# Kernel optimization log

Measured on AMD Instinct MI355X. Metric: run time of the kernel, lower is better.

The kernel has to match this reference:

```python
import jax, jax.numpy as jnp
import numpy as np

NG, K, LEN_KEEP = 128, 32, 32  # n_groups, group_size, int(128*(1-0.75))
ENC_HEADS, DEC_HEADS = 12, 16


def _fps(xyz, init, npoint):
    # iterative farthest point sampling; xyz (B,N,3), init (B,) start indices
    B, N, _ = xyz.shape
    def step(carry, _):
        dmin, far = carry
        c = jnp.take_along_axis(xyz, far[:, None, None], axis=1)  # (B,1,3)
        dmin = jnp.minimum(dmin, jnp.sum((xyz - c) ** 2, -1))
        return (dmin, jnp.argmax(dmin, -1)), far
    _, cents = jax.lax.scan(step, (jnp.full((B, N), 1e10, xyz.dtype), init), None, length=npoint)
    return cents.T  # (B, npoint)


def _knn(xyz, cents, k):
    # squared-distance knn (same ordering as euclidean cdist + topk smallest)
    x2 = jnp.sum(xyz * xyz, -1)          # (B,N)
    c2 = jnp.sum(cents * cents, -1)      # (B,M)
    d = c2[:, :, None] + x2[:, None, :] - 2.0 * jnp.einsum('bmc,bnc->bmn', cents, xyz)
    idx = jax.lax.top_k(-d, k)[1]        # (B,M,k)
    return jax.vmap(lambda p, i: p[i])(xyz, idx)  # (B,M,k,3)


def _bn(x, g, b):
    # train-mode BatchNorm1d over (batch, spatial), channel-last x (BM,k,C)
    m = x.mean((0, 1))
    v = x.var((0, 1))
    return (x - m) * jax.lax.rsqrt(v + 1e-5) * g + b


def _ln(x, g, b):
    m = x.mean(-1, keepdims=True)
    v = ((x - m) ** 2).mean(-1, keepdims=True)
    return (x - m) * jax.lax.rsqrt(v + 1e-5) * g + b


def _layer(x, qw, qb, ow, ob, l1g, l1b, f1w, f1b, f2w, f2b, l2g, l2b, nh):
    # post-norm TransformerEncoderLayer (relu FFN, no dropout = eval mode)
    B, S, D = x.shape
    dh = D // nh
    q, k, v = jnp.split(x @ qw.T + qb, 3, axis=-1)
    q = q.reshape(B, S, nh, dh); k = k.reshape(B, S, nh, dh); v = v.reshape(B, S, nh, dh)
    att = jax.nn.softmax(jnp.einsum('bqhd,bkhd->bhqk', q, k) * (1.0 / float(np.sqrt(dh))), axis=-1)
    o = jnp.einsum('bhqk,bkhd->bqhd', att, v).reshape(B, S, D) @ ow.T + ob
    x = _ln(x + o, l1g, l1b)
    f = jax.nn.relu(x @ f1w.T + f1b) @ f2w.T + f2b
    return _ln(x + f, l2g, l2b)


def _stack(x, qw, qb, ow, ob, l1g, l1b, f1w, f1b, f2w, f2b, l2g, l2b, nh):
    for i in range(qw.shape[0]):
        x = _layer(x, qw[i], qb[i], ow[i], ob[i], l1g[i], l1b[i], f1w[i], f1b[i], f2w[i], f2b[i], l2g[i], l2b[i], nh)
    return x


def _forward(xyz, fps_init, ids_shuffle, cw1, cb1, g1, be1, cw2, cb2, g2, be2, cw3, cb3, g3, be3, pos_w, pos_b, eqw, eqb, eow, eob, el1g, el1b, ef1w, ef1b, ef2w, ef2b, el2g, el2b, dew, deb, mtok, dpw, dpb, dqw, dqb, dow, dob, dl1g, dl1b, df1w, df1b, df2w, df2b, dl2g, dl2b, prw, prb):
    B = xyz.shape[0]
    cent_idx = _fps(xyz, fps_init, NG)
    cxyz = jax.vmap(lambda p, i: p[i])(xyz, cent_idx)      # (B,NG,3)
    gn = _knn(xyz, cxyz, K) - cxyz[:, :, None, :]          # (B,NG,K,3) centered groups
    h = gn.reshape(-1, K, 3)
    h = jax.nn.relu(_bn(h @ cw1.T + cb1, g1, be1))
    h = jax.nn.relu(_bn(h @ cw2.T + cb2, g2, be2))
    h = _bn(h @ cw3.T + cb3, g3, be3)
    tokens = h.max(axis=1).reshape(B, NG, -1)              # (B,NG,768)
    x = tokens + cxyz @ pos_w.T + pos_b
    ids_restore = jnp.argsort(ids_shuffle, axis=1)
    xk = jnp.take_along_axis(x, ids_shuffle[:, :LEN_KEEP, None], axis=1)
    mask = jnp.ones((B, NG), xyz.dtype).at[:, :LEN_KEEP].set(0.0)
    mask = jnp.take_along_axis(mask, ids_restore, axis=1)
    lat = _stack(xk, eqw, eqb, eow, eob, el1g, el1b, ef1w, ef1b, ef2w, ef2b, el2g, el2b, ENC_HEADS)
    y = lat @ dew.T + deb
    mt = jnp.broadcast_to(mtok, (B, NG - LEN_KEEP, mtok.shape[0]))
    y_ = jnp.take_along_axis(jnp.concatenate([y, mt], axis=1), ids_restore[:, :, None], axis=1)
    yd = y_ + cxyz @ dpw.T + dpb
    dec = _stack(yd, dqw, dqb, dow, dob, dl1g, dl1b, df1w, df1b, df2w, df2b, dl2g, dl2b, DEC_HEADS)
    pred = dec @ prw.T + prb                               # (B,NG,K*3)
    target = gn.reshape(B, NG, -1)                         # same FPS seed -> same centroids in loss branch
    l = ((pred - target) ** 2).mean(-1)
    loss = (l * mask).sum() / mask.sum()
    return loss, pred, mask


def setup_inputs():
    ks = iter(jax.random.split(jax.random.key(0), 64))
    def W(*shape):
        return jax.random.normal(next(ks), shape, jnp.float32) * 0.02
    B, N, D, DD, Le, Ld = 32, 8192, 768, 512, 12, 8
    d = {}
    d['xyz'] = jax.random.normal(next(ks), (B, N, 3), jnp.float32)
    d['fps_init'] = jax.random.randint(next(ks), (B,), 0, N)
    d['ids_shuffle'] = jnp.argsort(jax.random.uniform(next(ks), (B, NG)), axis=1)
    d['cw1'], d['cb1'], d['g1'], d['be1'] = W(64, 3), jnp.zeros(64), jnp.ones(64), jnp.zeros(64)
    d['cw2'], d['cb2'], d['g2'], d['be2'] = W(128, 64), jnp.zeros(128), jnp.ones(128), jnp.zeros(128)
    d['cw3'], d['cb3'], d['g3'], d['be3'] = W(D, 128), jnp.zeros(D), jnp.ones(D), jnp.zeros(D)
    d['pos_w'], d['pos_b'] = W(D, 3), jnp.zeros(D)
    d['eqw'], d['eqb'] = W(Le, 3 * D, D), jnp.zeros((Le, 3 * D))
    d['eow'], d['eob'] = W(Le, D, D), jnp.zeros((Le, D))
    d['el1g'], d['el1b'] = jnp.ones((Le, D)), jnp.zeros((Le, D))
    d['ef1w'], d['ef1b'] = W(Le, 4 * D, D), jnp.zeros((Le, 4 * D))
    d['ef2w'], d['ef2b'] = W(Le, D, 4 * D), jnp.zeros((Le, D))
    d['el2g'], d['el2b'] = jnp.ones((Le, D)), jnp.zeros((Le, D))
    d['dew'], d['deb'] = W(DD, D), jnp.zeros(DD)
    d['mtok'] = jnp.zeros(DD)
    d['dpw'], d['dpb'] = W(DD, 3), jnp.zeros(DD)
    d['dqw'], d['dqb'] = W(Ld, 3 * DD, DD), jnp.zeros((Ld, 3 * DD))
    d['dow'], d['dob'] = W(Ld, DD, DD), jnp.zeros((Ld, DD))
    d['dl1g'], d['dl1b'] = jnp.ones((Ld, DD)), jnp.zeros((Ld, DD))
    d['df1w'], d['df1b'] = W(Ld, 4 * DD, DD), jnp.zeros((Ld, 4 * DD))
    d['df2w'], d['df2b'] = W(Ld, DD, 4 * DD), jnp.zeros((Ld, DD))
    d['dl2g'], d['dl2b'] = jnp.ones((Ld, DD)), jnp.zeros((Ld, DD))
    d['prw'], d['prb'] = W(K * 3, DD), jnp.zeros(K * 3)
    return d


def reference(xyz, fps_init, ids_shuffle, cw1, cb1, g1, be1, cw2, cb2, g2, be2, cw3, cb3, g3, be3, pos_w, pos_b, eqw, eqb, eow, eob, el1g, el1b, ef1w, ef1b, ef2w, ef2b, el2g, el2b, dew, deb, mtok, dpw, dpb, dqw, dqb, dow, dob, dl1g, dl1b, df1w, df1b, df2w, df2b, dl2g, dl2b, prw, prb):
    return _forward(xyz, fps_init, ids_shuffle, cw1, cb1, g1, be1, cw2, cb2, g2, be2, cw3, cb3, g3, be3, pos_w, pos_b, eqw, eqb, eow, eob, el1g, el1b, ef1w, ef1b, ef2w, ef2b, el2g, el2b, dew, deb, mtok, dpw, dpb, dqw, dqb, dow, dob, dl1g, dl1b, df1w, df1b, df2w, df2b, dl2g, dl2b, prw, prb)
```

## Files before the change

### kernel.cpp

```cpp
#include <hip/hip_runtime.h>
#include <cmath>

#define BB 32
#define NPTS 8192
#define NG 128
#define KNB 32
#define LK 32
#define DE 768
#define DD 512
#define NLE 12
#define NLD 8

typedef __bf16 bf16x8 __attribute__((ext_vector_type(8)));
typedef float  f32x4  __attribute__((ext_vector_type(4)));
typedef unsigned long long u64;

#define WAITV(N) asm volatile("s_waitcnt vmcnt(" #N ")" ::: "memory")

static __device__ __forceinline__ bf16x8 pack8(float4 a, float4 b) {
    bf16x8 h;
    h[0] = (__bf16)a.x; h[1] = (__bf16)a.y; h[2] = (__bf16)a.z; h[3] = (__bf16)a.w;
    h[4] = (__bf16)b.x; h[5] = (__bf16)b.y; h[6] = (__bf16)b.z; h[7] = (__bf16)b.w;
    return h;
}

static __device__ __forceinline__ void gload16(const __bf16* g, __bf16* l) {
    __builtin_amdgcn_global_load_lds(
        (const __attribute__((address_space(1))) void*)g,
        (__attribute__((address_space(3))) void*)l,
        16, 0, 0);
}

static __device__ __forceinline__ unsigned fkey(float f) {
    unsigned u = __float_as_uint(f);
    return ((int)u < 0) ? ~u : (u | 0x80000000u);
}

__global__ __launch_bounds__(512, 1) void fps_kernel(
    const float* __restrict__ xyz, const int* __restrict__ init,
    float* __restrict__ cxyz)
{
#pragma clang fp contract(off)
    const int b = blockIdx.x;
    const float* P = xyz + (size_t)b * NPTS * 3;
    __shared__ float pxs[NPTS], pys[NPTS], pzs[NPTS];
    __shared__ u64 red[2][8];
    const int tid = threadIdx.x;
    float x[16], y[16], z[16], dmin[16];
    #pragma unroll
    for (int k = 0; k < 16; ++k) {
        int n = tid + (k << 9);
        float xx = P[n * 3 + 0], yy = P[n * 3 + 1], zz = P[n * 3 + 2];
        x[k] = xx; y[k] = yy; z[k] = zz;
        pxs[n] = xx; pys[n] = yy; pzs[n] = zz;
        dmin[k] = 1e10f;
    }
    int far = init[b];
    __syncthreads();
    for (int t = 0; t < NG; ++t) {
        float cx = pxs[far], cy = pys[far], cz = pzs[far];
        if (tid == 0) {
            cxyz[(b * NG + t) * 3 + 0] = cx;
            cxyz[(b * NG + t) * 3 + 1] = cy;
            cxyz[(b * NG + t) * 3 + 2] = cz;
        }
        float best = -1.0f; int bi = 0;
        #pragma unroll
        for (int k = 0; k < 16; ++k) {
            int n = tid + (k << 9);
            float dx = x[k] - cx, dy = y[k] - cy, dz = z[k] - cz;
            float d = dx * dx + dy * dy + dz * dz;
            float dm = dmin[k];
            if (d < dm) dm = d;
            dmin[k] = dm;
            if (dm > best) { best = dm; bi = n; }
        }
        u64 key = ((u64)__float_as_uint(best) << 32) | (unsigned)(8191 - bi);
        #pragma unroll
        for (int d = 32; d >= 1; d >>= 1) {
            u64 k2 = __shfl_down(key, d);
            if (k2 > key) key = k2;
        }
        if ((tid & 63) == 0) red[t & 1][tid >> 6] = key;
        __syncthreads();
        u64 kb = red[t & 1][0];
        #pragma unroll
        for (int w = 1; w < 8; ++w) {
            u64 k2 = red[t & 1][w];
            if (k2 > kb) kb = k2;
        }
        far = 8191 - (int)(kb & 0xFFFFFFFFu);
    }
}

__global__ __launch_bounds__(256) void knn_kernel(
    const float* __restrict__ xyz, const float* __restrict__ cxyz,
    float* __restrict__ gn)
{
#pragma clang fp contract(off)
    const int bm = blockIdx.x;
    const int b = bm / NG;
    const float* P = xyz + (size_t)b * NPTS * 3;
    __shared__ u64 cand[512];
    __shared__ u64 tmins[4];
    __shared__ int wcnt[4];
    __shared__ int order[KNB];
    const int tid = threadIdx.x;
    const int wv = tid >> 6, lane = tid & 63;
    const float cx = cxyz[bm * 3 + 0], cy = cxyz[bm * 3 + 1], cz = cxyz[bm * 3 + 2];
    const float c2 = cx * cx + cy * cy + cz * cz;
    unsigned fk[32];
    float bestf = 1e31f; int bi = 1 << 30;
    #pragma unroll
    for (int j = 0; j < 32; ++j) {
        int n = tid + (j << 8);
        float x = P[n * 3 + 0], y = P[n * 3 + 1], z = P[n * 3 + 2];
        float x2 = x * x + y * y + z * z;
        float dt = cx * x + cy * y + cz * z;
        float v = (c2 + x2) - 2.0f * dt;
        fk[j] = fkey(v);
        if (v < bestf) { bestf = v; bi = n; }
    }
    u64 mk = ((u64)fkey(bestf) << 32) | (unsigned)bi;
    {
        u64 v = mk;
        #pragma unroll
        for (int k = 2; k <= 64; k <<= 1) {
            #pragma unroll
            for (int j = k >> 1; j > 0; j >>= 1) {
                u64 o = __shfl_xor(v, j);
                bool up = ((lane & k) == 0);
                bool lower = ((lane & j) == 0);
                u64 mn = (v < o) ? v : o;
                u64 mx = (v < o) ? o : v;
                v = (up == lower) ? mn : mx;
            }
        }
        u64 Tw = __shfl(v, 31);
        if (lane == 0) tmins[wv] = Tw;
    }
    __syncthreads();
    u64 T = tmins[0];
    #pragma unroll
    for (int w = 1; w < 4; ++w) { u64 k2 = tmins[w]; if (k2 < T) T = k2; }
    int c = 0;
    #pragma unroll
    for (int j = 0; j < 32; ++j) {
        u64 key = ((u64)fk[j] << 32) | (unsigned)(tid + (j << 8));
        c += (key <= T) ? 1 : 0;
    }
    int s = c;
    #pragma unroll
    for (int d = 1; d < 64; d <<= 1) {
        int t2 = __shfl_up(s, d);
        if (lane >= d) s += t2;
    }
    int excl = s - c;
    if (lane == 63) wcnt[wv] = s;
    __syncthreads();
    int base = 0;
    for (int w = 0; w < wv; ++w) base += wcnt[w];
    int etot = wcnt[0] + wcnt[1] + wcnt[2] + wcnt[3];

    if (etot <= 512) {
        int pos = base + excl;
        #pragma unroll
        for (int j = 0; j < 32; ++j) {
            u64 key = ((u64)fk[j] << 32) | (unsigned)(tid + (j << 8));
            if (key <= T) cand[pos++] = key;
        }
        __syncthreads();
        for (int si = tid; si < etot; si += 256) {
            u64 my = cand[si];
            int r = 0;
            for (int j2 = 0; j2 < etot; ++j2) r += (cand[j2] < my) ? 1 : 0;
            if (r < KNB) order[r] = (int)(my & 0xFFFFFFFFu);
        }
        __syncthreads();
    } else {
        u64 bk = ~0ull;
        #pragma unroll
        for (int j = 0; j < 32; ++j) {
            u64 key = ((u64)fk[j] << 32) | (unsigned)(tid + (j << 8));
            if (key < bk) bk = key;
        }
        for (int r = 0; r < KNB; ++r) {
            u64 kk = bk;
            #pragma unroll
            for (int dd = 32; dd >= 1; dd >>= 1) {
                u64 k2 = __shfl_down(kk, dd);
                if (k2 < kk) kk = k2;
            }
            if (lane == 0) cand[(r & 1) * 4 + wv] = kk;
            __syncthreads();
            u64 kb = cand[(r & 1) * 4 + 0];
            #pragma unroll
            for (int w = 1; w < 4; ++w) { u64 k2 = cand[(r & 1) * 4 + w]; if (k2 < kb) kb = k2; }
            if (tid == 0) order[r] = (int)(kb & 0xFFFFFFFFu);
            if ((int)(kb & 255u) == tid) {
                int sj = (int)((kb & 0xFFFFFFFFu) >> 8);
                #pragma unroll
                for (int j = 0; j < 32; ++j) if (j == sj) fk[j] = 0xFFFFFFFFu;
                bk = ~0ull;
                #pragma unroll
                for (int j = 0; j < 32; ++j) {
                    u64 key = ((u64)fk[j] << 32) | (unsigned)(tid + (j << 8));
                    if (key < bk) bk = key;
                }
            }
            __syncthreads();
        }
    }
    if (tid < KNB) {
        int n = order[tid];
        gn[((size_t)bm * KNB + tid) * 3 + 0] = P[n * 3 + 0] - cx;
        gn[((size_t)bm * KNB + tid) * 3 + 1] = P[n * 3 + 1] - cy;
        gn[((size_t)bm * KNB + tid) * 3 + 2] = P[n * 3 + 2] - cz;
    }
}

__global__ void cvt_bf16_kernel(const float* __restrict__ src, __bf16* __restrict__ dst, int n8)
{
    int i = blockIdx.x * 256 + threadIdx.x;
    if (i >= n8) return;
    const float4* p = (const float4*)(src + (size_t)i * 8);
    *(bf16x8*)(dst + (size_t)i * 8) = pack8(p[0], p[1]);
}

struct CvtTab {
    const float* src[10];
    __bf16* dst[10];
    int cum[11];
};
__global__ void cvt_multi_kernel(CvtTab t)
{
    int i = blockIdx.x * 256 + threadIdx.x;
    if (i >= t.cum[10]) return;
    int seg = 0;
    #pragma unroll
    for (int k = 1; k < 10; ++k) seg += (i >= t.cum[k]) ? 1 : 0;
    int local = i - t.cum[seg];
    const float4* p = (const float4*)(t.src[seg] + (size_t)local * 8);
    *(bf16x8*)(t.dst[seg] + (size_t)local * 8) = pack8(p[0], p[1]);
}

__global__ void embed1_kernel(const float* __restrict__ gn, const float* __restrict__ w,
                              const float* __restrict__ bias, float* __restrict__ h1)
{
    int i = blockIdx.x * 256 + threadIdx.x;
    if (i >= 131072 * 64) return;
    int r = i >> 6, c = i & 63;
    const float* p = gn + (size_t)r * 3;
    h1[i] = p[0] * w[c * 3 + 0] + p[1] * w[c * 3 + 1] + p[2] * w[c * 3 + 2] + bias[c];
}

template <int C>
__global__ __launch_bounds__(256) void colstats_kernel(const float* __restrict__ X,
                                                       double* __restrict__ st, int Mrows)
{
    constexpr int RL = 256 / C;
    const int c = threadIdx.x % C;
    const int rl = threadIdx.x / C;
    double s = 0.0, s2 = 0.0;
    int rows_per_block = (Mrows + gridDim.x - 1) / gridDim.x;
    int r0 = blockIdx.x * rows_per_block;
    int r1 = min(r0 + rows_per_block, Mrows);
    for (int r = r0 + rl; r < r1; r += RL) {
        float v = X[(size_t)r * C + c];
        s += v; s2 += (double)v * v;
    }
    __shared__ double sh[2][256];
    sh[0][threadIdx.x] = s; sh[1][threadIdx.x] = s2;
    __syncthreads();
    if (rl == 0) {
        for (int j = 1; j < RL; ++j) { s += sh[0][j * C + c]; s2 += sh[1][j * C + c]; }
        atomicAdd(&st[c], s);
        atomicAdd(&st[C + c], s2);
    }
}

__global__ void bn_finalize(const double* __restrict__ st, const float* __restrict__ g,
                            const float* __restrict__ be, float* __restrict__ sc,
                            float* __restrict__ shb, int C)
{
    int c = blockIdx.x * 64 + threadIdx.x;
    if (c >= C) return;
    double m = st[c] / 131072.0;
    double var = st[C + c] / 131072.0 - m * m;
    if (var < 0.0) var = 0.0;
    float rs = rsqrtf((float)var + 1e-5f);
    sc[c] = rs * g[c];
    shb[c] = be[c] - (float)m * rs * g[c];
}

__global__ void bn_apply_bf16(const float* __restrict__ x, const float* __restrict__ sc,
                              const float* __restrict__ shb, __bf16* __restrict__ y,
                              int total, int C)
{
    int i = blockIdx.x * 256 + threadIdx.x;
    if (i >= total) return;
    int c = i % C;
    float v = x[i] * sc[c] + shb[c];
    v = fmaxf(v, 0.0f);
    y[i] = (__bf16)v;
}

template <int BM, int WM, int WN, int DEPTH>
__global__ __launch_bounds__(256) void gemm_bf16(
    const __bf16* __restrict__ A, const __bf16* __restrict__ W,
    const float* __restrict__ bias, float* __restrict__ Cf, __bf16* __restrict__ Cb,
    int M, int N, int K, int Kc, int relu)
{
    constexpr int MR = BM / WM / 16;
    constexpr int NR = 128 / WN / 16;
    constexpr int CA = BM * 8 / 256;
    __shared__ __bf16 As[DEPTH][BM * 64];
    __shared__ __bf16 Ws[DEPTH][128 * 64];
    const int tid = threadIdx.x;
    const int lane = tid & 63;
    const int wave = tid >> 6;
    const int wm = wave / WN, wn = wave % WN;
    const int m0 = blockIdx.y * BM, n0 = blockIdx.x * 128;
    const int kb = blockIdx.z * Kc;

    f32x4 acc[MR][NR] = {};

    auto stage = [&](int buf, int kt) {
        #pragma unroll
        for (int j = 0; j < CA; ++j) {
            int cb = j * 256 + (wave << 6);
            int c  = cb + lane;
            int row = c >> 3;
            int kcs = (c & 7) ^ (row & 7);
            gload16(A + (size_t)(m0 + row) * K + kb + kt + kcs * 8, &As[buf][cb * 8]);
        }
        #pragma unroll
        for (int j = 0; j < 4; ++j) {
            int cb = j * 256 + (wave << 6);
            int c  = cb + lane;
            int row = c >> 3;
            int kcs = (c & 7) ^ (row & 7);
            gload16(W + (size_t)(n0 + row) * K + kb + kt + kcs * 8, &Ws[buf][cb * 8]);
        }
    };
    auto compute = [&](int buf) {
        #pragma unroll
        for (int ks = 0; ks < 2; ++ks) {
            bf16x8 af[MR], bfr[NR];
            int kc = ks * 4 + (lane >> 4);
            #pragma unroll
            for (int i = 0; i < MR; ++i) {
                int rowA = wm * (BM / WM) + i * 16 + (lane & 15);
                af[i] = *(bf16x8*)&As[buf][rowA * 64 + ((kc ^ (rowA & 7)) * 8)];
            }
            #pragma unroll
            for (int j = 0; j < NR; ++j) {
                int rowB = wn * (128 / WN) + j * 16 + (lane & 15);
                bfr[j] = *(bf16x8*)&Ws[buf][rowB * 64 + ((kc ^ (rowB & 7)) * 8)];
            }
            #pragma unroll
            for (int i = 0; i < MR; ++i)
                #pragma unroll
                for (int j = 0; j < NR; ++j)
                    acc[i][j] = __builtin_amdgcn_mfma_f32_16x16x32_bf16(af[i], bfr[j], acc[i][j], 0, 0, 0);
        }
    };

    const int nt = Kc >> 6;
    stage(0, 0);
    if (DEPTH > 2 && nt > 1) stage(1, 64);
    for (int t = 0; t < nt; ++t) {
        int ahead = min(nt - 1, t + DEPTH - 2) - t;
        if (ahead >= 1) { if constexpr (BM == 64) WAITV(6); else WAITV(8); }
        else            WAITV(0);
        __syncthreads();
        if (t + DEPTH - 1 < nt) stage((t + DEPTH - 1) % DEPTH, (t + DEPTH - 1) << 6);
        compute(t % DEPTH);
    }

    float* Co = Cf ? Cf + (size_t)blockIdx.z * M * N : nullptr;
    #pragma unroll
    for (int j = 0; j < NR; ++j) {
        int col = n0 + wn * (128 / WN) + j * 16 + (lane & 15);
        if (col >= N) continue;
        float bv = (blockIdx.z == 0) ? bias[col] : 0.0f;
        #pragma unroll
        for (int i = 0; i < MR; ++i) {
            #pragma unroll
            for (int r = 0; r < 4; ++r) {
                int rowm = m0 + wm * (BM / WM) + i * 16 + (lane >> 4) * 4 + r;
                float v = acc[i][j][r] + bv;
                if (relu) v = fmaxf(v, 0.0f);
                if (Co) Co[(size_t)rowm * N + col] = v;
                if (Cb) Cb[(size_t)rowm * N + col] = (__bf16)v;
            }
        }
    }
}

__global__ __launch_bounds__(256) void embed3_mfma(
    const __bf16* __restrict__ A, const __bf16* __restrict__ W,
    const float* __restrict__ cb3,
    float* __restrict__ gmax, float* __restrict__ gmin, double* __restrict__ st3)
{
    __shared__ __bf16 As[2][128 * 64];
    __shared__ __bf16 Ws[2][128 * 64];
    const int tid = threadIdx.x;
    const int lane = tid & 63;
    const int wave = tid >> 6;
    const int wm = wave >> 1, wn = wave & 1;
    const int m0 = blockIdx.y * 128, n0 = blockIdx.x * 128;
    const int K = 128;

    f32x4 acc[4][4] = {};

    auto stage = [&](int buf, int kt) {
        #pragma unroll
        for (int j = 0; j < 4; ++j) {
            int cb = j * 256 + (wave << 6);
            int c  = cb + lane;
            int row = c >> 3;
            int kcs = (c & 7) ^ (row & 7);
            gload16(A + (size_t)(m0 + row) * K + kt + kcs * 8, &As[buf][cb * 8]);
            gload16(W + (size_t)(n0 + row) * K + kt + kcs * 8, &Ws[buf][cb * 8]);
        }
    };
    auto compute = [&](int buf) {
        #pragma unroll
        for (int ks = 0; ks < 2; ++ks) {
            bf16x8 af[4], bfr[4];
            int kc = ks * 4 + (lane >> 4);
            #pragma unroll
            for (int i = 0; i < 4; ++i) {
                int rowA = wm * 64 + i * 16 + (lane & 15);
                af[i] = *(bf16x8*)&As[buf][rowA * 64 + ((kc ^ (rowA & 7)) * 8)];
                int rowB = wn * 64 + i * 16 + (lane & 15);
                bfr[i] = *(bf16x8*)&Ws[buf][rowB * 64 + ((kc ^ (rowB & 7)) * 8)];
            }
            #pragma unroll
            for (int i = 0; i < 4; ++i)
                #pragma unroll
                for (int j = 0; j < 4; ++j)
                    acc[i][j] = __builtin_amdgcn_mfma_f32_16x16x32_bf16(af[i], bfr[j], acc[i][j], 0, 0, 0);
        }
    };

    stage(0, 0);
    stage(1, 64);
    WAITV(8);
    __syncthreads();
    compute(0);
    WAITV(0);
    __syncthreads();
    compute(1);

    #pragma unroll
    for (int j = 0; j < 4; ++j) {
        int col = n0 + wn * 64 + j * 16 + (lane & 15);
        float bv = cb3[col];
        float stot = 0.0f, s2tot = 0.0f;
        #pragma unroll
        for (int gi = 0; gi < 2; ++gi) {
            float mx = -1e30f, mn = 1e30f, s = 0.0f, s2 = 0.0f;
            #pragma unroll
            for (int ii = 0; ii < 2; ++ii) {
                f32x4 a = acc[gi * 2 + ii][j];
                #pragma unroll
                for (int r = 0; r < 4; ++r) {
                    float v = a[r] + bv;
                    mx = fmaxf(mx, v); mn = fminf(mn, v);
                    s += v; s2 += v * v;
                }
            }
            #pragma unroll
            for (int d = 16; d < 64; d <<= 1) {
                mx = fmaxf(mx, __shfl_xor(mx, d));
                mn = fminf(mn, __shfl_xor(mn, d));
                s  += __shfl_xor(s, d);
                s2 += __shfl_xor(s2, d);
            }
            stot += s; s2tot += s2;
            if (lane < 16) {
                int g = (m0 >> 5) + wm * 2 + gi;
                gmax[(size_t)g * 768 + col] = mx;
                gmin[(size_t)g * 768 + col] = mn;
            }
        }
        if (lane < 16) {
            double* stp = st3 + (size_t)(blockIdx.y & 31) * 1536;
            atomicAdd(&stp[col], (double)stot);
            atomicAdd(&stp[768 + col], (double)s2tot);
        }
    }
}

__global__ void bn3_finalize(const double* __restrict__ st3, const float* __restrict__ g,
                             const float* __restrict__ be, float* __restrict__ a3,
                             float* __restrict__ c3)
{
    int c = blockIdx.x * 256 + threadIdx.x;
    if (c >= 768) return;
    double s = 0.0, s2 = 0.0;
    for (int p = 0; p < 32; ++p) { s += st3[(size_t)p * 1536 + c]; s2 += st3[(size_t)p * 1536 + 768 + c]; }
    double m = s / 131072.0;
    double var = s2 / 131072.0 - m * m;
    if (var < 0.0) var = 0.0;
    float rs = rsqrtf((float)var + 1e-5f);
    a3[c] = rs * g[c];
    c3[c] = be[c] - (float)m * rs * g[c];
}

__global__ void tokens_pos(const float* __restrict__ gmax, const float* __restrict__ gmin,
                           const float* __restrict__ a3, const float* __restrict__ c3,
                           const float* __restrict__ cxyz, const float* __restrict__ posw,
                           const float* __restrict__ posb, const int* __restrict__ restore,
                           float* __restrict__ xe, __bf16* __restrict__ xeb)
{
    int i = blockIdx.x * 256 + threadIdx.x;
    if (i >= 4096 * 768) return;
    int c = i % 768, g = i / 768;
    int r = restore[g];
    if (r >= LK) return;
    float a = a3[c];
    float tok = (a >= 0.0f ? a * gmax[i] : a * gmin[i]) + c3[c];
    float px = cxyz[g * 3 + 0], py = cxyz[g * 3 + 1], pz = cxyz[g * 3 + 2];
    float v = tok + px * posw[c * 3 + 0] + py * posw[c * 3 + 1] + pz * posw[c * 3 + 2] + posb[c];
    int b = g >> 7;
    size_t idx = ((size_t)(b * LK + r)) * DE + c;
    xe[idx] = v;
    xeb[idx] = (__bf16)v;
}

__global__ void restore_kernel(const int* __restrict__ shuffle, int* __restrict__ restore,
                               float* __restrict__ maskv)
{
    int j = blockIdx.x * 256 + threadIdx.x;
    if (j >= BB * NG) return;
    int b = j / NG, p = j % NG;
    int dst = b * NG + shuffle[j];
    restore[dst] = p;
    maskv[dst] = (p < LK) ? 0.0f : 1.0f;
}

__global__ void yd_build(const float* __restrict__ ykp, const int* __restrict__ restore,
                         const float* __restrict__ mtok, const float* __restrict__ cxyz,
                         const float* __restrict__ dpw, const float* __restrict__ dpb,
                         float* __restrict__ xd, __bf16* __restrict__ xdb)
{
    const size_t PS = (size_t)1024 * DD;
    int i = blockIdx.x * 256 + threadIdx.x;
    if (i >= BB * NG * DD) return;
    int c = i % DD;
    int g = i / DD;
    int b = g / NG;
    int r = restore[g];
    float base;
    if (r < LK) {
        size_t o = (size_t)(b * LK + r) * DD + c;
        base = ykp[o] + ykp[PS + o] + ykp[2 * PS + o] + ykp[3 * PS + o];
    } else {
        base = mtok[c];
    }
    float px = cxyz[g * 3 + 0], py = cxyz[g * 3 + 1], pz = cxyz[g * 3 + 2];
    float v = base + px * dpw[c * 3 + 0] + py * dpw[c * 3 + 1] + pz * dpw[c * 3 + 2] + dpb[c];
    xd[i] = v;
    xdb[i] = (__bf16)v;
}

template <int S, int DH, int NH>
__global__ __launch_bounds__(256) void dattn_kernel(const __bf16* __restrict__ qkv,
                                                    __bf16* __restrict__ o, float scale)
{
    constexpr int D = NH * DH;
    constexpr int SQ = DH + 8;
    constexpr int SV = S + 8;
    __shared__ __bf16 Qb[S * SQ];
    __shared__ __bf16 Kb[S * SQ];
    __shared__ __bf16 Vt[DH * SV];
    __shared__ __bf16 Pb[S * SV];
    const int h = blockIdx.x % NH;
    const int b = blockIdx.x / NH;
    const int tid = threadIdx.x;
    const int lane = tid & 63, wv = tid >> 6;
    const __bf16* base = qkv + (size_t)b * S * 3 * D + h * DH;
    for (int i = tid; i < S * (DH / 8); i += 256) {
        int s = i / (DH / 8), c8 = (i % (DH / 8)) * 8;
        const __bf16* rp = base + (size_t)s * 3 * D;
        bf16x8 q = *(const bf16x8*)(rp + c8);
        bf16x8 k = *(const bf16x8*)(rp + D + c8);
        bf16x8 v = *(const bf16x8*)(rp + 2 * D + c8);
        *(bf16x8*)&Qb[s * SQ + c8] = q;
        *(bf16x8*)&Kb[s * SQ + c8] = k;
        #pragma unroll
        for (int j = 0; j < 8; ++j) Vt[(c8 + j) * SV + s] = v[j];
    }
    __syncthreads();
    const int q0 = wv * 32;
    const int arow = lane & 15;
    const int kch = (lane >> 4) * 8;
    const int rrow = (lane >> 4) * 4;
    f32x4 sc[2][8];
    {
        bf16x8 af0 = *(bf16x8*)&Qb[(q0 + arow) * SQ + kch];
        bf16x8 af1 = *(bf16x8*)&Qb[(q0 + 16 + arow) * SQ + kch];
        f32x4 z = {0.0f, 0.0f, 0.0f, 0.0f};
        #pragma unroll
        for (int j = 0; j < 8; ++j) {
            bf16x8 bf_ = *(bf16x8*)&Kb[(j * 16 + arow) * SQ + kch];
            sc[0][j] = __builtin_amdgcn_mfma_f32_16x16x32_bf16(af0, bf_, z, 0, 0, 0);
            sc[1][j] = __builtin_amdgcn_mfma_f32_16x16x32_bf16(af1, bf_, z, 0, 0, 0);
        }
    }
    #pragma unroll
    for (int i = 0; i < 2; ++i) {
        #pragma unroll
        for (int r = 0; r < 4; ++r) {
            float m = -1e30f;
            #pragma unroll
            for (int j = 0; j < 8; ++j) m = fmaxf(m, sc[i][j][r]);
            #pragma unroll
            for (int d = 8; d >= 1; d >>= 1) m = fmaxf(m, __shfl_xor(m, d));
            float sum = 0.0f;
            #pragma unroll
            for (int j = 0; j < 8; ++j) {
                float e = expf((sc[i][j][r] - m) * scale);
                sc[i][j][r] = e;
                sum += e;
            }
            #pragma unroll
            for (int d = 8; d >= 1; d >>= 1) sum += __shfl_xor(sum, d);
            float inv = 1.0f / sum;
            int row = q0 + i * 16 + rrow + r;
            #pragma unroll
            for (int j = 0; j < 8; ++j)
                Pb[row * SV + j * 16 + (lane & 15)] = (__bf16)(sc[i][j][r] * inv);
        }
    }
    #pragma unroll
    for (int i = 0; i < 2; ++i) {
        #pragma unroll
        for (int j2 = 0; j2 < 2; ++j2) {
            f32x4 a2 = {0.0f, 0.0f, 0.0f, 0.0f};
            #pragma unroll
            for (int ks = 0; ks < 4; ++ks) {
                bf16x8 pa = *(bf16x8*)&Pb[(q0 + i * 16 + arow) * SV + ks * 32 + kch];
                bf16x8 vb = *(bf16x8*)&Vt[(j2 * 16 + arow) * SV + ks * 32 + kch];
                a2 = __builtin_amdgcn_mfma_f32_16x16x32_bf16(pa, vb, a2, 0, 0, 0);
            }
            #pragma unroll
            for (int r = 0; r < 4; ++r) {
                int q = q0 + i * 16 + rrow + r;
                o[((size_t)(b * S + q)) * D + h * DH + j2 * 16 + (lane & 15)] = (__bf16)a2[r];
            }
        }
    }
}

template <int S, int DH, int NH>
__global__ __launch_bounds__(64) void eattn_kernel(const __bf16* __restrict__ qkv,
                                                   __bf16* __restrict__ o, float scale)
{
    constexpr int D = NH * DH;
    constexpr int SQ = DH + 8;
    constexpr int SV = S + 8;
    __shared__ __bf16 Qb[S * SQ];
    __shared__ __bf16 Kb[S * SQ];
    __shared__ __bf16 Vt[DH * SV];
    __shared__ __bf16 Pb[S * SV];
    const int h = blockIdx.x % NH;
    const int b = blockIdx.x / NH;
    const int lane = threadIdx.x;
    const __bf16* base = qkv + (size_t)b * S * 3 * D + h * DH;
    for (int i = lane; i < S * (DH / 8); i += 64) {
        int s = i / (DH / 8), c8 = (i % (DH / 8)) * 8;
        const __bf16* rp = base + (size_t)s * 3 * D;
        bf16x8 q = *(const bf16x8*)(rp + c8);
        bf16x8 k = *(const bf16x8*)(rp + D + c8);
        bf16x8 v = *(const bf16x8*)(rp + 2 * D + c8);
        *(bf16x8*)&Qb[s * SQ + c8] = q;
        *(bf16x8*)&Kb[s * SQ + c8] = k;
        #pragma unroll
        for (int j = 0; j < 8; ++j) Vt[(c8 + j) * SV + s] = v[j];
    }
    __syncthreads();
    const int arow = lane & 15;
    const int kch = (lane >> 4) * 8;
    const int rrow = (lane >> 4) * 4;
    f32x4 sc[2][2] = {};
    #pragma unroll
    for (int ks = 0; ks < 2; ++ks) {
        bf16x8 af0 = *(bf16x8*)&Qb[(arow) * SQ + ks * 32 + kch];
        bf16x8 af1 = *(bf16x8*)&Qb[(16 + arow) * SQ + ks * 32 + kch];
        #pragma unroll
        for (int j = 0; j < 2; ++j) {
            bf16x8 bf_ = *(bf16x8*)&Kb[(j * 16 + arow) * SQ + ks * 32 + kch];
            sc[0][j] = __builtin_amdgcn_mfma_f32_16x16x32_bf16(af0, bf_, sc[0][j], 0, 0, 0);
            sc[1][j] = __builtin_amdgcn_mfma_f32_16x16x32_bf16(af1, bf_, sc[1][j], 0, 0, 0);
        }
    }
    #pragma unroll
    for (int i = 0; i < 2; ++i) {
        #pragma unroll
        for (int r = 0; r < 4; ++r) {
            float m = fmaxf(sc[i][0][r], sc[i][1][r]);
            #pragma unroll
            for (int d = 8; d >= 1; d >>= 1) m = fmaxf(m, __shfl_xor(m, d));
            float sum = 0.0f;
            #pragma unroll
            for (int j = 0; j < 2; ++j) {
                float e = expf((sc[i][j][r] - m) * scale);
                sc[i][j][r] = e;
                sum += e;
            }
            #pragma unroll
            for (int d = 8; d >= 1; d >>= 1) sum += __shfl_xor(sum, d);
            float inv = 1.0f / sum;
            int row = i * 16 + rrow + r;
            #pragma unroll
            for (int j = 0; j < 2; ++j)
                Pb[row * SV + j * 16 + (lane & 15)] = (__bf16)(sc[i][j][r] * inv);
        }
    }
    __syncthreads();
    #pragma unroll
    for (int i = 0; i < 2; ++i) {
        bf16x8 pa = *(bf16x8*)&Pb[(i * 16 + arow) * SV + kch];
        #pragma unroll
        for (int j2 = 0; j2 < 4; ++j2) {
            bf16x8 vb = *(bf16x8*)&Vt[(j2 * 16 + arow) * SV + kch];
            f32x4 z = {0.0f, 0.0f, 0.0f, 0.0f};
            f32x4 a2 = __builtin_amdgcn_mfma_f32_16x16x32_bf16(pa, vb, z, 0, 0, 0);
            #pragma unroll
            for (int r = 0; r < 4; ++r) {
                int q = i * 16 + rrow + r;
                o[((size_t)(b * S + q)) * D + h * DH + j2 * 16 + (lane & 15)] = (__bf16)a2[r];
            }
        }
    }
}

template <int D, int SK>
__global__ __launch_bounds__(256) void ln_res(float* __restrict__ x, const float* __restrict__ part,
                                              size_t pstride,
                                              const float* __restrict__ g, const float* __restrict__ b,
                                              __bf16* __restrict__ xb)
{
    constexpr int J = D / 256;
    __shared__ float pr[2][4];
    const size_t off = (size_t)blockIdx.x * D;
    const int tid = threadIdx.x;
    float vals[J];
    float s = 0.0f, s2 = 0.0f;
    #pragma unroll
    for (int j = 0; j < J; ++j) {
        int i = tid + j * 256;
        float v = x[off + i];
        #pragma unroll
        for (int sk = 0; sk < SK; ++sk) v += part[(size_t)sk * pstride + off + i];
        vals[j] = v; s += v; s2 += v * v;
    }
    #pragma unroll
    for (int d = 32; d >= 1; d >>= 1) { s += __shfl_down(s, d); s2 += __shfl_down(s2, d); }
    if ((tid & 63) == 0) { pr[0][tid >> 6] = s; pr[1][tid >> 6] = s2; }
    __syncthreads();
    float st = pr[0][0] + pr[0][1] + pr[0][2] + pr[0][3];
    float s2t = pr[1][0] + pr[1][1] + pr[1][2] + pr[1][3];
    float m = st / D;
    float var = s2t / D - m * m;
    if (var < 0.0f) var = 0.0f;
    float rs = rsqrtf(var + 1e-5f);
    #pragma unroll
    for (int j = 0; j < J; ++j) {
        int i = tid + j * 256;
        float v = (vals[j] - m) * rs * g[i] + b[i];
        x[off + i] = v;
        xb[off + i] = (__bf16)v;
    }
}

__global__ __launch_bounds__(128) void loss_l(const float* __restrict__ predp,
                                              const float* __restrict__ target,
                                              const float* __restrict__ maskv,
                                              float* __restrict__ pred_out,
                                              float* __restrict__ lm)
{
    const size_t PS = (size_t)4096 * 96;
    const int g = blockIdx.x;
    __shared__ float red[128];
    int t = threadIdx.x;
    float s = 0.0f;
    if (t < 96) {
        size_t o = (size_t)g * 96 + t;
        float v = predp[o] + predp[PS + o] + predp[2 * PS + o] + predp[3 * PS + o];
        pred_out[o] = v;
        float d = v - target[o];
        s = d * d;
    }
    red[t] = s; __syncthreads();
    for (int st = 64; st > 0; st >>= 1) { if (t < st) red[t] += red[t + st]; __syncthreads(); }
    if (t == 0) lm[g] = (red[0] / 96.0f) * maskv[g];
}

__global__ __launch_bounds__(1024) void loss_final(const float* __restrict__ lm,
                                                   const float* __restrict__ maskv,
                                                   float* __restrict__ out)
{
    __shared__ float r1[1024], r2[1024];
    int t = threadIdx.x;
    float a = 0.0f, b = 0.0f;
    for (int i = t; i < BB * NG; i += 1024) { a += lm[i]; b += maskv[i]; }
    r1[t] = a; r2[t] = b; __syncthreads();
    for (int st = 512; st > 0; st >>= 1) { if (t < st) { r1[t] += r1[t + st]; r2[t] += r2[t + st]; } __syncthreads(); }
    if (t == 0) out[0] = r1[0] / r2[0];
}

extern "C" void kernel_launch(void* const* d_in, const int* in_sizes, int n_in,
                              void* d_out, int out_size, void* d_ws, size_t ws_size,
                              hipStream_t stream)
{
    (void)in_sizes; (void)n_in; (void)out_size; (void)ws_size;
    const float* xyz        = (const float*)d_in[0];
    const int*   fps_init   = (const int*)d_in[1];
    const int*   ids_shuf   = (const int*)d_in[2];
    const float* cw1 = (const float*)d_in[3];  const float* cb1 = (const float*)d_in[4];
    const float* g1  = (const float*)d_in[5];  const float* be1 = (const float*)d_in[6];
    const float* cw2 = (const float*)d_in[7];  const float* cb2 = (const float*)d_in[8];
    const float* g2  = (const float*)d_in[9];  const float* be2 = (const float*)d_in[10];
    const float* cw3 = (const float*)d_in[11]; const float* cb3 = (const float*)d_in[12];
    const float* g3  = (const float*)d_in[13]; const float* be3 = (const float*)d_in[14];
    const float* posw = (const float*)d_in[15]; const float* posb = (const float*)d_in[16];
    const float* eqw = (const float*)d_in[17]; const float* eqb = (const float*)d_in[18];
    const float* eow = (const float*)d_in[19]; const float* eob = (const float*)d_in[20];
    const float* el1g = (const float*)d_in[21]; const float* el1b = (const float*)d_in[22];
    const float* ef1w = (const float*)d_in[23]; const float* ef1b = (const float*)d_in[24];
    const float* ef2w = (const float*)d_in[25]; const float* ef2b = (const float*)d_in[26];
    const float* el2g = (const float*)d_in[27]; const float* el2b = (const float*)d_in[28];
    const float* dew = (const float*)d_in[29]; const float* deb = (const float*)d_in[30];
    const float* mtok = (const float*)d_in[31];
    const float* dpw = (const float*)d_in[32]; const float* dpb = (const float*)d_in[33];
    const float* dqw = (const float*)d_in[34]; const float* dqb = (const float*)d_in[35];
    const float* dow = (const float*)d_in[36]; const float* dob = (const float*)d_in[37];
    const float* dl1g = (const float*)d_in[38]; const float* dl1b = (const float*)d_in[39];
    const float* df1w = (const float*)d_in[40]; const float* df1b = (const float*)d_in[41];
    const float* df2w = (const float*)d_in[42]; const float* df2b = (const float*)d_in[43];
    const float* dl2g = (const float*)d_in[44]; const float* dl2b = (const float*)d_in[45];
    const float* prw = (const float*)d_in[46]; const float* prb = (const float*)d_in[47];
    float* out = (float*)d_out;
    float* pred = out + 1;
    float* maskv = out + 1 + (size_t)BB * NG * KNB * 3;

    char* ws = (char*)d_ws;
    size_t off = 0;
    auto alloc = [&](size_t bytes) -> void* {
        void* p = ws + off;
        off = (off + bytes + 255) & ~(size_t)255;
        return p;
    };
    double* st1 = (double*)alloc(128 * 8);
    double* st2 = (double*)alloc(256 * 8);
    double* st3 = (double*)alloc((size_t)32 * 1536 * 8);
    float* sc1 = (float*)alloc(64 * 4);  float* sh1 = (float*)alloc(64 * 4);
    float* sc2 = (float*)alloc(128 * 4); float* sh2 = (float*)alloc(128 * 4);
    float* a3 = (float*)alloc(768 * 4);  float* c3 = (float*)alloc(768 * 4);
    int* restore = (int*)alloc(4096 * 4);
    float* cxyz = (float*)alloc(12288 * 4);
    float* gn   = (float*)alloc((size_t)393216 * 4);
    __bf16* cw2b = (__bf16*)alloc((size_t)128 * 64 * 2);
    __bf16* cw3b = (__bf16*)alloc((size_t)768 * 128 * 2);
    float* xfull = (float*)alloc((size_t)4096 * 768 * 4);
    float* xe    = (float*)alloc((size_t)1024 * 768 * 4);
    __bf16* xeb  = (__bf16*)alloc((size_t)1024 * 768 * 2);
    float* qkve  = (float*)alloc((size_t)1024 * 2304 * 4);
    __bf16* qkveb = (__bf16*)alloc((size_t)1024 * 2304 * 2);
    __bf16* oeb  = (__bf16*)alloc((size_t)1024 * 768 * 2);
    __bf16* fe1b = (__bf16*)alloc((size_t)1024 * 3072 * 2);
    float* xd    = (float*)alloc((size_t)4096 * 512 * 4);
    __bf16* xdb  = (__bf16*)alloc((size_t)4096 * 512 * 2);
    float* qkvd  = (float*)alloc((size_t)4096 * 1536 * 4);
    __bf16* qkvdb = (__bf16*)alloc((size_t)4096 * 1536 * 2);
    __bf16* odb  = (__bf16*)alloc((size_t)4096 * 512 * 2);
    __bf16* fd1b = (__bf16*)alloc((size_t)4096 * 2048 * 2);
    float* lm    = (float*)alloc(4096 * 4);

    __bf16* eqwb  = (__bf16*)alloc((size_t)NLE * 3 * DE * DE * 2);
    __bf16* eowb  = (__bf16*)alloc((size_t)NLE * DE * DE * 2);
    __bf16* ef1wb = (__bf16*)alloc((size_t)NLE * 4 * DE * DE * 2);
    __bf16* ef2wb = (__bf16*)alloc((size_t)NLE * 4 * DE * DE * 2);
    __bf16* dewb  = (__bf16*)alloc((size_t)DD * DE * 2);
    __bf16* dqwb  = (__bf16*)alloc((size_t)NLD * 3 * DD * DD * 2);
    __bf16* dowb  = (__bf16*)alloc((size_t)NLD * DD * DD * 2);
    __bf16* df1wb = (__bf16*)alloc((size_t)NLD * 4 * DD * DD * 2);
    __bf16* df2wb = (__bf16*)alloc((size_t)NLD * 4 * DD * DD * 2);
    __bf16* prwb  = (__bf16*)alloc((size_t)128 * 512 * 2);

    char* U = (char*)eqwb;
    float*  h1   = (float*)U;
    __bf16* h1b  = (__bf16*)(U + (size_t)33554432);
    float*  h2   = (float*)(U + (size_t)50331648);
    __bf16* h2b  = (__bf16*)(U + (size_t)117440512);
    float* gmax = qkvd;
    float* gmin = qkvd + (size_t)3145728;
    float* predp = (float*)fd1b;

    size_t stats_bytes = (size_t)((char*)st3 + (size_t)32 * 1536 * 8 - (char*)st1);
    hipMemsetAsync((void*)st1, 0, stats_bytes, stream);

    auto cvt = [&](const float* src, __bf16* dst, size_t n) {
        int n8 = (int)(n / 8);
        cvt_bf16_kernel<<<(n8 + 255) / 256, 256, 0, stream>>>(src, dst, n8);
    };
    auto gemm = [&](const __bf16* A, const __bf16* Wt, const float* bias,
                    float* Cf, __bf16* Cb, int M, int N, int K, int relu) {
        int nb128 = ((N + 127) / 128) * (M / 128);
        if (nb128 < 256) {
            dim3 grid((N + 127) / 128, M / 64, 1);
            gemm_bf16<64, 1, 4, 3><<<grid, 256, 0, stream>>>(A, Wt, bias, Cf, Cb, M, N, K, K, relu);
        } else {
            dim3 grid((N + 127) / 128, M / 128, 1);
            gemm_bf16<128, 2, 2, 2><<<grid, 256, 0, stream>>>(A, Wt, bias, Cf, Cb, M, N, K, K, relu);
        }
    };
    auto gemmSK = [&](const __bf16* A, const __bf16* Wt, const float* bias,
                      float* Cf, int M, int N, int K, int SK) {
        dim3 grid((N + 127) / 128, M / 64, SK);
        gemm_bf16<64, 1, 4, 3><<<grid, 256, 0, stream>>>(A, Wt, bias, Cf, nullptr, M, N, K, K / SK, 0);
    };

    cvt(cw2, cw2b, 128 * 64);
    cvt(cw3, cw3b, 768 * 128);

    fps_kernel<<<BB, 512, 0, stream>>>(xyz, fps_init, cxyz);
    knn_kernel<<<BB * NG, 256, 0, stream>>>(xyz, cxyz, gn);

    embed1_kernel<<<(131072 * 64 + 255) / 256, 256, 0, stream>>>(gn, cw1, cb1, h1);
    colstats_kernel<64><<<256, 256, 0, stream>>>(h1, st1, 131072);
    bn_finalize<<<1, 64, 0, stream>>>(st1, g1, be1, sc1, sh1, 64);
    bn_apply_bf16<<<(131072 * 64 + 255) / 256, 256, 0, stream>>>(h1, sc1, sh1, h1b, 131072 * 64, 64);
    gemm(h1b, cw2b, cb2, h2, nullptr, 131072, 128, 64, 0);
    colstats_kernel<128><<<256, 256, 0, stream>>>(h2, st2, 131072);
    bn_finalize<<<2, 64, 0, stream>>>(st2, g2, be2, sc2, sh2, 128);
    bn_apply_bf16<<<(131072 * 128 + 255) / 256, 256, 0, stream>>>(h2, sc2, sh2, h2b, 131072 * 128, 128);
    embed3_mfma<<<dim3(6, 1024), 256, 0, stream>>>(h2b, cw3b, cb3, gmax, gmin, st3);
    bn3_finalize<<<3, 256, 0, stream>>>(st3, g3, be3, a3, c3);

    restore_kernel<<<16, 256, 0, stream>>>(ids_shuf, restore, maskv);
    tokens_pos<<<(4096 * 768 + 255) / 256, 256, 0, stream>>>(gmax, gmin, a3, c3, cxyz, posw, posb,
                                                             restore, xe, xeb);

    {
        CvtTab t;
        const float* srcs[10] = {eqw, eow, ef1w, ef2w, dew, dqw, dow, df1w, df2w, prw};
        __bf16* dsts[10] = {eqwb, eowb, ef1wb, ef2wb, dewb, dqwb, dowb, df1wb, df2wb, prwb};
        size_t ns[10] = {
            (size_t)NLE * 3 * DE * DE, (size_t)NLE * DE * DE,
            (size_t)NLE * 4 * DE * DE, (size_t)NLE * 4 * DE * DE,
            (size_t)DD * DE,
            (size_t)NLD * 3 * DD * DD, (size_t)NLD * DD * DD,
            (size_t)NLD * 4 * DD * DD, (size_t)NLD * 4 * DD * DD,
            (size_t)96 * 512
        };
        int cum = 0;
        t.cum[0] = 0;
        for (int k = 0; k < 10; ++k) {
            t.src[k] = srcs[k]; t.dst[k] = dsts[k];
            cum += (int)(ns[k] / 8);
            t.cum[k + 1] = cum;
        }
        cvt_multi_kernel<<<(cum + 255) / 256, 256, 0, stream>>>(t);
        hipMemsetAsync((void*)(prwb + (size_t)96 * 512), 0, (size_t)32 * 512 * 2, stream);
    }

    const size_t PSE = (size_t)1024 * DE;
    const size_t PSD = (size_t)4096 * DD;

    for (int l = 0; l < NLE; ++l) {
        gemm(xeb, eqwb + (size_t)l * 3 * DE * DE, eqb + (size_t)l * 3 * DE, nullptr, qkveb, 1024, 3 * DE, DE, 0);
        eattn_kernel<LK, 64, 12><<<BB * 12, 64, 0, stream>>>(qkveb, oeb, 0.125f);
        gemmSK(oeb, eowb + (size_t)l * DE * DE, eob + (size_t)l * DE, xfull, 1024, DE, DE, 4);
        ln_res<DE, 4><<<BB * LK, 256, 0, stream>>>(xe, xfull, PSE, el1g + (size_t)l * DE, el1b + (size_t)l * DE, xeb);
        gemm(xeb, ef1wb + (size_t)l * 4 * DE * DE, ef1b + (size_t)l * 4 * DE, nullptr, fe1b, 1024, 4 * DE, DE, 1);
        gemmSK(fe1b, ef2wb + (size_t)l * DE * 4 * DE, ef2b + (size_t)l * DE, xfull, 1024, DE, 4 * DE, 4);
        ln_res<DE, 4><<<BB * LK, 256, 0, stream>>>(xe, xfull, PSE, el2g + (size_t)l * DE, el2b + (size_t)l * DE, xeb);
    }

    gemmSK(xeb, dewb, deb, qkve, 1024, DD, DE, 4);
    yd_build<<<(BB * NG * DD + 255) / 256, 256, 0, stream>>>(qkve, restore, mtok, cxyz, dpw, dpb, xd, xdb);

    const float dsc = (float)(1.0 / sqrt(32.0));
    for (int l = 0; l < NLD; ++l) {
        gemm(xdb, dqwb + (size_t)l * 3 * DD * DD, dqb + (size_t)l * 3 * DD, nullptr, qkvdb, 4096, 3 * DD, DD, 0);
        dattn_kernel<NG, 32, 16><<<BB * 16, 256, 0, stream>>>(qkvdb, odb, dsc);
        gemmSK(odb, dowb + (size_t)l * DD * DD, dob + (size_t)l * DD, qkvd, 4096, DD, DD, 2);
        ln_res<DD, 2><<<BB * NG, 256, 0, stream>>>(xd, qkvd, PSD, dl1g + (size_t)l * DD, dl1b + (size_t)l * DD, xdb);
        gemm(xdb, df1wb + (size_t)l * 4 * DD * DD, df1b + (size_t)l * 4 * DD, nullptr, fd1b, 4096, 4 * DD, DD, 1);
        gemmSK(fd1b, df2wb + (size_t)l * DD * 4 * DD, df2b + (size_t)l * DD, qkvd, 4096, DD, 4 * DD, 2);
        ln_res<DD, 2><<<BB * NG, 256, 0, stream>>>(xd, qkvd, PSD, dl2g + (size_t)l * DD, dl2b + (size_t)l * DD, xdb);
    }

    gemmSK(xdb, prwb, prb, predp, 4096, 96, 512, 4);
    loss_l<<<BB * NG, 128, 0, stream>>>(predp, gn, maskv, pred, lm);
    loss_final<<<1, 1024, 0, stream>>>(lm, maskv, out);
}
```

Baseline: 2.376 ms.

## Fuse BN2 column statistics into conv2 GEMM epilogue with spread atomics

Adds a STATS template flag to the bf16 GEMM so the conv2 GEMM epilogue accumulates per-column sum and sum-of-squares. These are reduced across lanes with shuffles and added atomically into 32 spread double buffers, which a new finalize kernel then sums. This removes the separate colstats pass that re-read the 131072x128 fp32 h2 tensor. It also raises the threshold for choosing the 64-row GEMM tile from 256 to 400 blocks, which changes tile selection for the transformer GEMMs.

```diff
diff --git a/kernel.cpp b/kernel.cpp
--- a/kernel.cpp
+++ b/kernel.cpp
@@ -293,6 +293,25 @@
     shb[c] = be[c] - (float)m * rs * g[c];
 }
 
+__global__ void bn_spread_finalize(const double* __restrict__ st, const float* __restrict__ g,
+                                   const float* __restrict__ be, float* __restrict__ sc,
+                                   float* __restrict__ shb, int C)
+{
+    int c = blockIdx.x * 64 + threadIdx.x;
+    if (c >= C) return;
+    double s = 0.0, s2 = 0.0;
+    for (int p = 0; p < 32; ++p) {
+        s  += st[(size_t)p * 2 * C + c];
+        s2 += st[(size_t)p * 2 * C + C + c];
+    }
+    double m = s / 131072.0;
+    double var = s2 / 131072.0 - m * m;
+    if (var < 0.0) var = 0.0;
+    float rs = rsqrtf((float)var + 1e-5f);
+    sc[c] = rs * g[c];
+    shb[c] = be[c] - (float)m * rs * g[c];
+}
+
 __global__ void bn_apply_bf16(const float* __restrict__ x, const float* __restrict__ sc,
                               const float* __restrict__ shb, __bf16* __restrict__ y,
                               int total, int C)
@@ -305,11 +324,11 @@
     y[i] = (__bf16)v;
 }
 
-template <int BM, int WM, int WN, int DEPTH>
+template <int BM, int WM, int WN, int DEPTH, bool STATS>
 __global__ __launch_bounds__(256) void gemm_bf16(
     const __bf16* __restrict__ A, const __bf16* __restrict__ W,
     const float* __restrict__ bias, float* __restrict__ Cf, __bf16* __restrict__ Cb,
-    int M, int N, int K, int Kc, int relu)
+    int M, int N, int K, int Kc, int relu, double* __restrict__ st)
 {
     constexpr int MR = BM / WM / 16;
     constexpr int NR = 128 / WN / 16;
@@ -384,6 +403,7 @@
         int col = n0 + wn * (128 / WN) + j * 16 + (lane & 15);
         if (col >= N) continue;
         float bv = (blockIdx.z == 0) ? bias[col] : 0.0f;
+        float s = 0.0f, s2 = 0.0f;
         #pragma unroll
         for (int i = 0; i < MR; ++i) {
             #pragma unroll
@@ -391,8 +411,21 @@
                 int rowm = m0 + wm * (BM / WM) + i * 16 + (lane >> 4) * 4 + r;
                 float v = acc[i][j][r] + bv;
                 if (relu) v = fmaxf(v, 0.0f);
+                if (STATS) { s += v; s2 += v * v; }
                 if (Co) Co[(size_t)rowm * N + col] = v;
                 if (Cb) Cb[(size_t)rowm * N + col] = (__bf16)v;
+            }
+        }
+        if constexpr (STATS) {
+            #pragma unroll
+            for (int d = 16; d < 64; d <<= 1) {
+                s  += __shfl_xor(s, d);
+                s2 += __shfl_xor(s2, d);
+            }
+            if (lane < 16) {
+                double* stp = st + (size_t)(blockIdx.y & 31) * 2 * 128;
+                atomicAdd(&stp[col], (double)s);
+                atomicAdd(&stp[128 + col], (double)s2);
             }
         }
     }
@@ -857,7 +890,7 @@
         return p;
     };
     double* st1 = (double*)alloc(128 * 8);
-    double* st2 = (double*)alloc(256 * 8);
+    double* st2 = (double*)alloc((size_t)32 * 256 * 8);
     double* st3 = (double*)alloc((size_t)32 * 1536 * 8);
     float* sc1 = (float*)alloc(64 * 4);  float* sh1 = (float*)alloc(64 * 4);
     float* sc2 = (float*)alloc(128 * 4); float* sh2 = (float*)alloc(128 * 4);
@@ -912,18 +945,18 @@
     auto gemm = [&](const __bf16* A, const __bf16* Wt, const float* bias,
                     float* Cf, __bf16* Cb, int M, int N, int K, int relu) {
         int nb128 = ((N + 127) / 128) * (M / 128);
-        if (nb128 < 256) {
+        if (nb128 < 400) {
             dim3 grid((N + 127) / 128, M / 64, 1);
-            gemm_bf16<64, 1, 4, 3><<<grid, 256, 0, stream>>>(A, Wt, bias, Cf, Cb, M, N, K, K, relu);
+            gemm_bf16<64, 1, 4, 3, false><<<grid, 256, 0, stream>>>(A, Wt, bias, Cf, Cb, M, N, K, K, relu, nullptr);
         } else {
             dim3 grid((N + 127) / 128, M / 128, 1);
-            gemm_bf16<128, 2, 2, 2><<<grid, 256, 0, stream>>>(A, Wt, bias, Cf, Cb, M, N, K, K, relu);
+            gemm_bf16<128, 2, 2, 2, false><<<grid, 256, 0, stream>>>(A, Wt, bias, Cf, Cb, M, N, K, K, relu, nullptr);
         }
     };
     auto gemmSK = [&](const __bf16* A, const __bf16* Wt, const float* bias,
                       float* Cf, int M, int N, int K, int SK) {
         dim3 grid((N + 127) / 128, M / 64, SK);
-        gemm_bf16<64, 1, 4, 3><<<grid, 256, 0, stream>>>(A, Wt, bias, Cf, nullptr, M, N, K, K / SK, 0);
+        gemm_bf16<64, 1, 4, 3, false><<<grid, 256, 0, stream>>>(A, Wt, bias, Cf, nullptr, M, N, K, K / SK, 0, nullptr);
     };
 
     cvt(cw2, cw2b, 128 * 64);
@@ -936,9 +969,9 @@
     colstats_kernel<64><<<256, 256, 0, stream>>>(h1, st1, 131072);
     bn_finalize<<<1, 64, 0, stream>>>(st1, g1, be1, sc1, sh1, 64);
     bn_apply_bf16<<<(131072 * 64 + 255) / 256, 256, 0, stream>>>(h1, sc1, sh1, h1b, 131072 * 64, 64);
-    gemm(h1b, cw2b, cb2, h2, nullptr, 131072, 128, 64, 0);
-    colstats_kernel<128><<<256, 256, 0, stream>>>(h2, st2, 131072);
-    bn_finalize<<<2, 64, 0, stream>>>(st2, g2, be2, sc2, sh2, 128);
+    gemm_bf16<128, 2, 2, 2, true><<<dim3(1, 1024, 1), 256, 0, stream>>>(
+        h1b, cw2b, cb2, h2, nullptr, 131072, 128, 64, 64, 0, st2);
+    bn_spread_finalize<<<2, 64, 0, stream>>>(st2, g2, be2, sc2, sh2, 128);
     bn_apply_bf16<<<(131072 * 128 + 255) / 256, 256, 0, stream>>>(h2, sc2, sh2, h2b, 131072 * 128, 128);
     embed3_mfma<<<dim3(6, 1024), 256, 0, stream>>>(h2b, cw3b, cb3, gmax, gmin, st3);
     bn3_finalize<<<3, 256, 0, stream>>>(st3, g3, be3, a3, c3);
```

Result: no change. 2.340 ms (-1.5%).
